# Kernel tuning notes

Measured on AMD Instinct MI355X. Metric: run time of the kernel, lower is better.

## Reference

```python
import jax, jax.numpy as jnp
import numpy as np

B, S, H, E, K, NH = 2, 2048, 1024, 8, 2, 8
HD = H // NH          # head dim = 128
HQ = H // 4           # seasonal encoder width = 256
CAP = int(B * S * 1.5 * K / E)  # expert capacity = 1536


def setup_inputs() -> dict:
    key = jax.random.key(0)
    ks = iter(jax.random.split(key, 32))

    def lin(shape):
        fan_in = shape[0]
        return jax.random.normal(next(ks), shape, jnp.float32) / np.sqrt(fan_in)

    inp = {
        "hidden_states": jax.random.normal(next(ks), (B, S, H), jnp.float32),
        # position embedding table [sequence_length, H]
        "pos_emb": jax.random.normal(next(ks), (S, H), jnp.float32) * 0.02,
        # temporal_encoder: Linear(H+2,H) -> ReLU -> Linear(H,H)
        "We1": lin((H + 2, H)), "be1": jnp.zeros((H,), jnp.float32),
        "We2": lin((H, H)),     "be2": jnp.zeros((H,), jnp.float32),
        # seasonal_encoder: Linear(1,H//4) -> ReLU -> Linear(H//4,H//4)
        "Ws1": lin((1, HQ)),   "bs1": jnp.zeros((HQ,), jnp.float32),
        "Ws2": lin((HQ, HQ)),  "bs2": jnp.zeros((HQ,), jnp.float32),
        # temporal_attention (MultiheadAttention, 8 heads)
        "Wq": lin((H, H)), "bq": jnp.zeros((H,), jnp.float32),
        "Wk": lin((H, H)), "bk": jnp.zeros((H,), jnp.float32),
        "Wv": lin((H, H)), "bv": jnp.zeros((H,), jnp.float32),
        "Wo": lin((H, H)), "bo": jnp.zeros((H,), jnp.float32),
        # temporal_router: Linear(H,H) -> ReLU -> Linear(H,E)
        "Wr1": lin((H, H)), "br1": jnp.zeros((H,), jnp.float32),
        "Wr2": lin((H, E)), "br2": jnp.zeros((E,), jnp.float32),
    }
    return inp


def _forward(hidden_states, pos_emb, We1, be1, We2, be2, Ws1, bs1, Ws2, bs2,
             Wq, bq, Wk, bk, Wv, bv, Wo, bo, Wr1, br1, Wr2, br2):
    b, s, h = hidden_states.shape
    # time features (time_info is None -> defaults)
    t = jnp.arange(s, dtype=jnp.float32)                   # [S]
    season = jnp.sin(t * 2.0 * jnp.pi / 24.0)              # [S]
    time_feat = jnp.broadcast_to(jnp.stack([t, season], -1), (b, s, 2))

    combined = jnp.concatenate([hidden_states, time_feat], axis=-1)  # [B,S,H+2]
    enc = jax.nn.relu(combined @ We1 + be1) @ We2 + be2              # [B,S,H]

    pos = pos_emb[:s]                                                # [S,H]
    seas = jax.nn.relu(season[:, None] @ Ws1 + bs1) @ Ws2 + bs2      # [S,H//4]
    seas_full = jnp.tile(seas, (1, h // seas.shape[-1]))             # [S,H] (expand to H)

    x = enc + pos[None] + seas_full[None]                            # [B,S,H]

    # self-attention (eval mode, no dropout)
    def heads(y):
        return y.reshape(b, s, NH, HD)
    q = heads(x @ Wq + bq)
    k = heads(x @ Wk + bk)
    v = heads(x @ Wv + bv)
    scores = jnp.einsum('bqhd,bkhd->bhqk', q, k) / np.sqrt(HD)
    attn = jax.nn.softmax(scores, axis=-1)
    ctx = jnp.einsum('bhqk,bkhd->bqhd', attn, v).reshape(b, s, h)
    x = ctx @ Wo + bo

    logits = jax.nn.relu(x @ Wr1 + br1) @ Wr2 + br2                  # [B,S,E]
    probs = jax.nn.softmax(logits, axis=-1)

    topv, topi = jax.lax.top_k(probs, K)                             # [B,S,K]
    topv = topv / topv.sum(-1, keepdims=True)

    onehot = jax.nn.one_hot(topi, E, dtype=probs.dtype)              # [B,S,K,E]
    disp0 = onehot.sum(-2)                                           # [B,S,E] (0/1)
    comb0 = (topv[..., None] * onehot).sum(-2)                       # [B,S,E]

    # only capacity slot 0 is ever written (per original code)
    dispatch = jnp.zeros((b, s, E, CAP), probs.dtype).at[..., 0].set(disp0)
    combine = jnp.zeros((b, s, E, CAP), probs.dtype).at[..., 0].set(comb0)

    p_mean = probs.mean(axis=(0, 1))                                 # [E]
    aux_loss = jnp.sum(p_mean * jnp.log(p_mean * E + 1e-9))
    return dispatch, combine, probs, aux_loss


def reference(hidden_states, pos_emb, We1, be1, We2, be2, Ws1, bs1, Ws2, bs2,
              Wq, bq, Wk, bk, Wv, bv, Wo, bo, Wr1, br1, Wr2, br2):
    return _forward(hidden_states, pos_emb, We1, be1, We2, be2, Ws1, bs1, Ws2, bs2,
                    Wq, bq, Wk, bk, Wv, bv, Wo, bo, Wr1, br1, Wr2, br2)
```

## Files before the change

### kernel.cpp

```cpp
#include <hip/hip_runtime.h>
#include <hip/hip_fp16.h>
#include <math.h>

#define N_TOK 4096
#define S_LEN 2048
#define H_DIM 1024
#define E_EXP 8
#define CAPV  1536
#define NHEAD 8
#define HDHD  128

typedef __attribute__((ext_vector_type(8))) _Float16 v8h;
typedef __attribute__((ext_vector_type(4))) float v4f;

__device__ __forceinline__ void splitf16(float v, unsigned short& h, unsigned short& l) {
    __half hh = __float2half(v);
    h = __half_as_ushort(hh);
    l = __half_as_ushort(__float2half(v - __half2float(hh)));
}

__device__ __forceinline__ void gld_lds16(const void* g, void* l) {
    __builtin_amdgcn_global_load_lds(
        (const __attribute__((address_space(1))) unsigned int*)g,
        (__attribute__((address_space(3))) unsigned int*)l,
        16, 0, 0);
}

__global__ void season_k(float* seasons) {
    int s = blockIdx.x * 256 + threadIdx.x;
    if (s < S_LEN) {
        double a = (double)s * 2.0 * M_PI / 24.0;
        seasons[s] = (float)sin(a);
    }
}

__global__ void seas24_k(const float* __restrict__ seasons,
                         const float* __restrict__ Ws1, const float* __restrict__ bs1,
                         const float* __restrict__ Ws2, const float* __restrict__ bs2,
                         float* __restrict__ seas24) {
    __shared__ float hbuf[256];
    int m = blockIdx.x;
    float sv = seasons[m];
    int j = threadIdx.x;
    hbuf[j] = fmaxf(sv * Ws1[j] + bs1[j], 0.f);
    __syncthreads();
    float acc = bs2[j];
    for (int i = 0; i < 256; ++i) acc = fmaf(hbuf[i], Ws2[i * 256 + j], acc);
    seas24[m * 256 + j] = acc;
}

__global__ void wr2t_k(const float* __restrict__ Wr2, float* __restrict__ Wr2T) {
    int i = blockIdx.x * 256 + threadIdx.x;
    int k = i >> 3, e = i & 7;
    Wr2T[e * 1024 + k] = Wr2[i];
}

__global__ void convert_split_k(const float* __restrict__ in,
                                unsigned short* __restrict__ hi,
                                unsigned short* __restrict__ lo, int n4) {
    int i = blockIdx.x * 256 + threadIdx.x;
    if (i >= n4) return;
    float4 v = ((const float4*)in)[i];
    ushort4 h, l;
    splitf16(v.x, h.x, l.x);
    splitf16(v.y, h.y, l.y);
    splitf16(v.z, h.z, l.z);
    splitf16(v.w, h.w, l.w);
    ((ushort4*)hi)[i] = h;
    ((ushort4*)lo)[i] = l;
}

__device__ __forceinline__ void wconv_body(const float* __restrict__ W,
                                           unsigned short* __restrict__ Thi,
                                           unsigned short* __restrict__ Tlo) {
    __shared__ unsigned short Hs[64][65];
    __shared__ unsigned short Ls[64][65];
    int k0 = blockIdx.y * 64, n0 = blockIdx.x * 64;
    int tid = threadIdx.x;
#pragma unroll
    for (int i = 0; i < 4; ++i) {
        int idx = tid + i * 256;
        int kk = idx >> 4, n4 = idx & 15;
        float4 v = *(const float4*)(W + (size_t)(k0 + kk) * 1024 + n0 + n4 * 4);
        unsigned short h, l;
        splitf16(v.x, h, l); Hs[n4 * 4 + 0][kk] = h; Ls[n4 * 4 + 0][kk] = l;
        splitf16(v.y, h, l); Hs[n4 * 4 + 1][kk] = h; Ls[n4 * 4 + 1][kk] = l;
        splitf16(v.z, h, l); Hs[n4 * 4 + 2][kk] = h; Ls[n4 * 4 + 2][kk] = l;
        splitf16(v.w, h, l); Hs[n4 * 4 + 3][kk] = h; Ls[n4 * 4 + 3][kk] = l;
    }
    __syncthreads();
#pragma unroll
    for (int i = 0; i < 4; ++i) {
        int idx = tid + i * 256;
        int n = idx >> 4, k4 = idx & 15;
        ushort4 h = make_ushort4(Hs[n][k4 * 4], Hs[n][k4 * 4 + 1], Hs[n][k4 * 4 + 2], Hs[n][k4 * 4 + 3]);
        ushort4 l = make_ushort4(Ls[n][k4 * 4], Ls[n][k4 * 4 + 1], Ls[n][k4 * 4 + 2], Ls[n][k4 * 4 + 3]);
        *(ushort4*)(Thi + (size_t)(n0 + n) * 1024 + k0 + k4 * 4) = h;
        *(ushort4*)(Tlo + (size_t)(n0 + n) * 1024 + k0 + k4 * 4) = l;
    }
}

__global__ __launch_bounds__(256) void wconv_t_k(const float* __restrict__ W,
                                                 unsigned short* __restrict__ Thi,
                                                 unsigned short* __restrict__ Tlo) {
    wconv_body(W, Thi, Tlo);
}

struct WBatch {
    const float* src[7];
    unsigned short* dh[7];
    unsigned short* dl[7];
};

__global__ __launch_bounds__(256) void wconv_batch_k(WBatch wb) {
    int i = blockIdx.z;
    wconv_body(wb.src[i], wb.dh[i], wb.dl[i]);
}

template <int MODE, int EMITF, int EMITS, int EMITT>
__global__ __launch_bounds__(256, 2) void gemm_split(
    const unsigned short* __restrict__ Ahi, const unsigned short* __restrict__ Alo,
    const unsigned short* __restrict__ WThi, const unsigned short* __restrict__ WTlo,
    const float* __restrict__ bias, float* __restrict__ Cf,
    unsigned short* __restrict__ Chi, unsigned short* __restrict__ Clo,
    const float* __restrict__ rowT, const float* __restrict__ rowS,
    const float* __restrict__ seasons, const float* __restrict__ pos,
    const float* __restrict__ seas24, float escale) {
    __shared__ unsigned short Ash[2][128 * 32];
    __shared__ unsigned short Asl[2][128 * 32];
    __shared__ unsigned short Bsh[2][64 * 32];
    __shared__ unsigned short Bsl[2][64 * 32];
    int tid = threadIdx.x;
    int lane = tid & 63, w = tid >> 6;
    int l15 = lane & 15, l16 = lane >> 4;
    int wm = (w >> 1) * 64, wn = (w & 1) * 32;
    int m0 = blockIdx.y * 128, n0 = blockIdx.x * 64;

    int ac0 = w * 128 + lane;
    int ac1 = ac0 + 64;
    int bc  = w * 64 + lane;
    int ar0 = ac0 >> 2, ar1 = ac1 >> 2, bn = bc >> 2;
    size_t a_src0 = (size_t)(m0 + ar0) * 1024 + (((ac0 & 3) ^ (ar0 & 3)) * 8);
    size_t a_src1 = (size_t)(m0 + ar1) * 1024 + (((ac1 & 3) ^ (ar1 & 3)) * 8);
    size_t b_src  = (size_t)(n0 + bn) * 1024 + (((bc & 3) ^ (bn & 3)) * 8);

    int a_off[4], b_off[2];
#pragma unroll
    for (int mi = 0; mi < 4; ++mi) {
        int row = wm + mi * 16 + l15;
        a_off[mi] = row * 32 + ((l16 ^ (row & 3)) * 8);
    }
#pragma unroll
    for (int ni = 0; ni < 2; ++ni) {
        int n = wn + ni * 16 + l15;
        b_off[ni] = n * 32 + ((l16 ^ (n & 3)) * 8);
    }

    auto STAGE = [&](int buf, int k0) {
        gld_lds16(Ahi + a_src0 + k0, &Ash[buf][ac0 * 8]);
        gld_lds16(Ahi + a_src1 + k0, &Ash[buf][ac1 * 8]);
        gld_lds16(Alo + a_src0 + k0, &Asl[buf][ac0 * 8]);
        gld_lds16(Alo + a_src1 + k0, &Asl[buf][ac1 * 8]);
        gld_lds16(WThi + b_src + k0, &Bsh[buf][bc * 8]);
        gld_lds16(WTlo + b_src + k0, &Bsl[buf][bc * 8]);
    };

    v4f acc[4][2] = {};
    STAGE(0, 0);
    __syncthreads();

    for (int kk = 0; kk < 32; ++kk) {
        int cur = kk & 1;
        if (kk < 31) STAGE(cur ^ 1, (kk + 1) * 32);
        v8h ah[4], al[4], bh[2], bl[2];
#pragma unroll
        for (int mi = 0; mi < 4; ++mi) {
            ah[mi] = *(const v8h*)&Ash[cur][a_off[mi]];
            al[mi] = *(const v8h*)&Asl[cur][a_off[mi]];
        }
#pragma unroll
        for (int ni = 0; ni < 2; ++ni) {
            bh[ni] = *(const v8h*)&Bsh[cur][b_off[ni]];
            bl[ni] = *(const v8h*)&Bsl[cur][b_off[ni]];
        }
#pragma unroll
        for (int mi = 0; mi < 4; ++mi)
#pragma unroll
            for (int ni = 0; ni < 2; ++ni) {
                acc[mi][ni] = __builtin_amdgcn_mfma_f32_16x16x32_f16(ah[mi], bh[ni], acc[mi][ni], 0, 0, 0);
                acc[mi][ni] = __builtin_amdgcn_mfma_f32_16x16x32_f16(al[mi], bh[ni], acc[mi][ni], 0, 0, 0);
                acc[mi][ni] = __builtin_amdgcn_mfma_f32_16x16x32_f16(ah[mi], bl[ni], acc[mi][ni], 0, 0, 0);
            }
        __syncthreads();
    }

    if (EMITT) {
#pragma unroll
        for (int mi = 0; mi < 4; ++mi) {
            int row0 = m0 + wm + mi * 16 + l16 * 4;
            int bb = row0 >> 11, ss = row0 & 2047;
#pragma unroll
            for (int ni = 0; ni < 2; ++ni) {
                int col = n0 + wn + ni * 16 + l15;
                int hh = col >> 7, dd = col & 127;
                size_t base = ((size_t)((bb * 8 + hh) * 128 + dd)) * 2048 + ss;
                ushort4 vh, vl;
                float v0 = acc[mi][ni][0] + bias[col];
                float v1 = acc[mi][ni][1] + bias[col];
                float v2 = acc[mi][ni][2] + bias[col];
                float v3 = acc[mi][ni][3] + bias[col];
                splitf16(v0, vh.x, vl.x);
                splitf16(v1, vh.y, vl.y);
                splitf16(v2, vh.z, vl.z);
                splitf16(v3, vh.w, vl.w);
                *(ushort4*)(Chi + base) = vh;
                *(ushort4*)(Clo + base) = vl;
            }
        }
    } else {
#pragma unroll
        for (int mi = 0; mi < 4; ++mi) {
#pragma unroll
            for (int r = 0; r < 4; ++r) {
                int row = m0 + wm + mi * 16 + l16 * 4 + r;
                int s = row & (S_LEN - 1);
                float tval = 0.f, seval = 0.f;
                if (MODE == 1) { tval = (float)s; seval = seasons[s]; }
#pragma unroll
                for (int ni = 0; ni < 2; ++ni) {
                    int col = n0 + wn + ni * 16 + l15;
                    float v = acc[mi][ni][r] + bias[col];
                    if (MODE == 1) v += tval * rowT[col] + seval * rowS[col];
                    if (MODE == 2) v += pos[(size_t)s * 1024 + col] + seas24[(s % 24) * 256 + (col & 255)];
                    if (MODE == 1 || MODE == 3) v = fmaxf(v, 0.f);
                    size_t o = (size_t)row * 1024 + col;
                    if (EMITF) Cf[o] = v;
                    if (EMITS) {
                        unsigned short hu, lu;
                        splitf16(v * escale, hu, lu);
                        Chi[o] = hu; Clo[o] = lu;
                    }
                }
            }
        }
    }
}

#define ATTN_LDS_BYTES (4 * 2 * 4096 * 2 + 64 * 32 * 4)

__global__ __launch_bounds__(256, 2) void attn_mfma_k(
    const unsigned short* __restrict__ qhi, const unsigned short* __restrict__ qlo,
    const unsigned short* __restrict__ khi, const unsigned short* __restrict__ klo,
    const unsigned short* __restrict__ vthi, const unsigned short* __restrict__ vtlo,
    unsigned short* __restrict__ ctx_hi, unsigned short* __restrict__ ctx_lo) {
    extern __shared__ char smem_raw[];
    unsigned short* Ks_hi = (unsigned short*)smem_raw;
    unsigned short* Ks_lo = Ks_hi + 2 * 4096;
    unsigned short* Vs_hi = Ks_lo + 2 * 4096;
    unsigned short* Vs_lo = Vs_hi + 2 * 4096;
    unsigned int*   Ps    = (unsigned int*)(Vs_lo + 2 * 4096);

    int bh = blockIdx.y;
    int b = bh >> 3, h = bh & 7;
    int q0 = blockIdx.x * 64;
    int tid = threadIdx.x;
    int lane = tid & 63, w = tid >> 6;
    int l15 = lane & 15, l16 = lane >> 4;
    int wm = w * 16;

    v8h qa_h[4], qa_l[4];
    {
        size_t qrow = (size_t)(b * S_LEN + q0 + wm + l15) * H_DIM + h * HDHD;
#pragma unroll
        for (int ks = 0; ks < 4; ++ks) {
            qa_h[ks] = *(const v8h*)(qhi + qrow + ks * 32 + l16 * 8);
            qa_l[ks] = *(const v8h*)(qlo + qrow + ks * 32 + l16 * 8);
        }
    }

    int ktok1 = tid >> 4, kslot1 = tid & 15;
    int ktok2 = ktok1 + 16;
    size_t ksrc1 = (size_t)(b * S_LEN + ktok1) * H_DIM + h * HDHD + ((kslot1 ^ (ktok1 & 7)) * 8);
    size_t ksrc2 = (size_t)(b * S_LEN + ktok2) * H_DIM + h * HDHD + ((kslot1 ^ (ktok2 & 7)) * 8);
    int vd1 = tid >> 2, vslot1 = tid & 3;
    int vd2 = vd1 + 64;
    size_t vsrc1 = (size_t)(bh * HDHD + vd1) * S_LEN + ((vslot1 ^ ((vd1 >> 1) & 3)) * 8);
    size_t vsrc2 = (size_t)(bh * HDHD + vd2) * S_LEN + ((vslot1 ^ ((vd2 >> 1) & 3)) * 8);

    auto STAGE = [&](int buf, int kt) {
        size_t koff = (size_t)kt * H_DIM;
        int o = buf * 4096;
        gld_lds16(khi + ksrc1 + koff, &Ks_hi[o + tid * 8]);
        gld_lds16(khi + ksrc2 + koff, &Ks_hi[o + (tid + 256) * 8]);
        gld_lds16(klo + ksrc1 + koff, &Ks_lo[o + tid * 8]);
        gld_lds16(klo + ksrc2 + koff, &Ks_lo[o + (tid + 256) * 8]);
        gld_lds16(vthi + vsrc1 + kt, &Vs_hi[o + tid * 8]);
        gld_lds16(vthi + vsrc2 + kt, &Vs_hi[o + (tid + 256) * 8]);
        gld_lds16(vtlo + vsrc1 + kt, &Vs_lo[o + tid * 8]);
        gld_lds16(vtlo + vsrc2 + kt, &Vs_lo[o + (tid + 256) * 8]);
    };

    v4f accO[8] = {};
    float mreg[4] = {-1e30f, -1e30f, -1e30f, -1e30f};
    float lreg[4] = {};

    STAGE(0, 0);
    __syncthreads();

    for (int it = 0; it < 64; ++it) {
        int cur = it & 1;
        int co = cur * 4096;
        if (it < 63) STAGE(cur ^ 1, (it + 1) * 32);

        v4f s0 = {}, s1 = {};
#pragma unroll
        for (int ks = 0; ks < 4; ++ks) {
#pragma unroll
            for (int nt = 0; nt < 2; ++nt) {
                int tok = nt * 16 + l15;
                int slot = (ks * 4 + l16) ^ (tok & 7);
                v8h bhf = *(const v8h*)&Ks_hi[co + tok * 128 + slot * 8];
                v8h blf = *(const v8h*)&Ks_lo[co + tok * 128 + slot * 8];
                v4f& ss = nt ? s1 : s0;
                ss = __builtin_amdgcn_mfma_f32_16x16x32_f16(qa_h[ks], bhf, ss, 0, 0, 0);
                ss = __builtin_amdgcn_mfma_f32_16x16x32_f16(qa_l[ks], bhf, ss, 0, 0, 0);
                ss = __builtin_amdgcn_mfma_f32_16x16x32_f16(qa_h[ks], blf, ss, 0, 0, 0);
            }
        }

        float p0[4], p1[4], alpha[4];
#pragma unroll
        for (int r = 0; r < 4; ++r) {
            float tmax = fmaxf(s0[r], s1[r]);
            tmax = fmaxf(tmax, __shfl_xor(tmax, 1));
            tmax = fmaxf(tmax, __shfl_xor(tmax, 2));
            tmax = fmaxf(tmax, __shfl_xor(tmax, 4));
            tmax = fmaxf(tmax, __shfl_xor(tmax, 8));
            float mnew = fmaxf(mreg[r], tmax);
            alpha[r] = __expf(mreg[r] - mnew);
            p0[r] = __expf(s0[r] - mnew);
            p1[r] = __expf(s1[r] - mnew);
            float lt = p0[r] + p1[r];
            lt += __shfl_xor(lt, 1);
            lt += __shfl_xor(lt, 2);
            lt += __shfl_xor(lt, 4);
            lt += __shfl_xor(lt, 8);
            lreg[r] = lreg[r] * alpha[r] + lt;
            mreg[r] = mnew;
        }
#pragma unroll
        for (int nt = 0; nt < 8; ++nt)
#pragma unroll
            for (int r = 0; r < 4; ++r) accO[nt][r] *= alpha[r];

#pragma unroll
        for (int r = 0; r < 4; ++r) {
            int qq = wm + l16 * 4 + r;
            unsigned short ph, pl;
            splitf16(p0[r], ph, pl);
            int k0i = l15;
            Ps[qq * 32 + ((((k0i >> 2) ^ (qq & 7)) << 2) | (k0i & 3))] =
                (unsigned)ph | ((unsigned)pl << 16);
            splitf16(p1[r], ph, pl);
            int k1i = 16 + l15;
            Ps[qq * 32 + ((((k1i >> 2) ^ (qq & 7)) << 2) | (k1i & 3))] =
                (unsigned)ph | ((unsigned)pl << 16);
        }

        int qq = wm + l15;
        int sA = (l16 * 2) ^ (qq & 7);
        int sB = (l16 * 2 + 1) ^ (qq & 7);
        uint4 ua = *(const uint4*)&Ps[qq * 32 + sA * 4];
        uint4 ub = *(const uint4*)&Ps[qq * 32 + sB * 4];
        uint4 ahw, alw;
        ahw.x = (ua.x & 0xffffu) | (ua.y << 16);
        ahw.y = (ua.z & 0xffffu) | (ua.w << 16);
        ahw.z = (ub.x & 0xffffu) | (ub.y << 16);
        ahw.w = (ub.z & 0xffffu) | (ub.w << 16);
        alw.x = (ua.x >> 16) | (ua.y & 0xffff0000u);
        alw.y = (ua.z >> 16) | (ua.w & 0xffff0000u);
        alw.z = (ub.x >> 16) | (ub.y & 0xffff0000u);
        alw.w = (ub.z >> 16) | (ub.w & 0xffff0000u);
        v8h pA_h = __builtin_bit_cast(v8h, ahw);
        v8h pA_l = __builtin_bit_cast(v8h, alw);
#pragma unroll
        for (int nt = 0; nt < 8; ++nt) {
            int d = nt * 16 + l15;
            int slot = l16 ^ ((d >> 1) & 3);
            v8h vhf = *(const v8h*)&Vs_hi[co + d * 32 + slot * 8];
            v8h vlf = *(const v8h*)&Vs_lo[co + d * 32 + slot * 8];
            accO[nt] = __builtin_amdgcn_mfma_f32_16x16x32_f16(pA_h, vhf, accO[nt], 0, 0, 0);
            accO[nt] = __builtin_amdgcn_mfma_f32_16x16x32_f16(pA_l, vhf, accO[nt], 0, 0, 0);
            accO[nt] = __builtin_amdgcn_mfma_f32_16x16x32_f16(pA_h, vlf, accO[nt], 0, 0, 0);
        }
        __syncthreads();
    }

    float linv[4];
#pragma unroll
    for (int r = 0; r < 4; ++r) linv[r] = 1.f / lreg[r];
#pragma unroll
    for (int nt = 0; nt < 8; ++nt) {
#pragma unroll
        for (int r = 0; r < 4; ++r) {
            size_t o = (size_t)(b * S_LEN + q0 + wm + l16 * 4 + r) * H_DIM + h * HDHD + nt * 16 + l15;
            unsigned short hu, lu;
            splitf16(accO[nt][r] * linv[r], hu, lu);
            ctx_hi[o] = hu;
            ctx_lo[o] = lu;
        }
    }
}

__global__ __launch_bounds__(256) void logits_k(const float* __restrict__ h1,
                                                const float* __restrict__ Wr2T,
                                                const float* __restrict__ br2,
                                                float* __restrict__ logits) {
    __shared__ float part[256];
    int tid = threadIdx.x;
    int tok8 = tid >> 5;
    int e = (tid >> 2) & 7;
    int ch = tid & 3;
    int tok = blockIdx.x * 8 + tok8;
    const float4* h4 = (const float4*)(h1 + (size_t)tok * 1024 + ch * 256);
    const float4* w4 = (const float4*)(Wr2T + (size_t)e * 1024 + ch * 256);
    float acc = 0.f;
#pragma unroll
    for (int i = 0; i < 64; ++i) {
        float4 a = h4[i];
        float4 bb = w4[i];
        acc = fmaf(a.x, bb.x, fmaf(a.y, bb.y, fmaf(a.z, bb.z, fmaf(a.w, bb.w, acc))));
    }
    part[tid] = acc;
    __syncthreads();
    if (ch == 0) {
        float s = part[tid] + part[tid + 1] + part[tid + 2] + part[tid + 3] + br2[e];
        logits[(size_t)tok * 8 + e] = s;
    }
}

__global__ __launch_bounds__(256) void topk_fill_k(const float* __restrict__ logits,
                                                   float* __restrict__ out) {
    int tok = blockIdx.x;
    int tid = threadIdx.x;
    float l[8], p[8];
    float mx = -1e30f;
#pragma unroll
    for (int e = 0; e < 8; ++e) { l[e] = logits[(size_t)tok * 8 + e]; mx = fmaxf(mx, l[e]); }
    float sum = 0.f;
#pragma unroll
    for (int e = 0; e < 8; ++e) { p[e] = __expf(l[e] - mx); sum += p[e]; }
    float inv = 1.f / sum;
#pragma unroll
    for (int e = 0; e < 8; ++e) p[e] *= inv;
    int i1 = 0;
#pragma unroll
    for (int e = 1; e < 8; ++e) if (p[e] > p[i1]) i1 = e;
    int i2 = -1;
#pragma unroll
    for (int e = 0; e < 8; ++e) {
        if (e == i1) continue;
        if (i2 < 0 || p[e] > p[i2]) i2 = e;
    }
    float tv = p[i1] + p[i2];
    float w1 = p[i1] / tv, w2 = p[i2] / tv;

    const size_t NEC = (size_t)N_TOK * E_EXP * CAPV;
    v4f* dbase = (v4f*)(out + (size_t)tok * E_EXP * CAPV);
    v4f* cbase = (v4f*)(out + NEC + (size_t)tok * E_EXP * CAPV);
    const int NF4 = E_EXP * CAPV / 4;
#pragma unroll
    for (int it = 0; it < NF4 / 256; ++it) {
        int f = it * 256 + tid;
        int e = f / (CAPV / 4);
        int c4 = f - e * (CAPV / 4);
        v4f dv = {0.f, 0.f, 0.f, 0.f};
        v4f cv = {0.f, 0.f, 0.f, 0.f};
        if (c4 == 0) {
            if (e == i1) { dv[0] = 1.f; cv[0] = w1; }
            else if (e == i2) { dv[0] = 1.f; cv[0] = w2; }
        }
        __builtin_nontemporal_store(dv, dbase + f);
        __builtin_nontemporal_store(cv, cbase + f);
    }
    if (tid < 2) {
        float4 pv = tid == 0 ? make_float4(p[0], p[1], p[2], p[3])
                             : make_float4(p[4], p[5], p[6], p[7]);
        ((float4*)(out + 2 * NEC + (size_t)tok * 8))[tid] = pv;
    }
}

__global__ void aux_k(const float* __restrict__ probs, float* __restrict__ out_aux) {
    __shared__ float part[256];
    int tid = threadIdx.x;
    int e = tid & 7, chunk = tid >> 3;
    float s = 0.f;
    for (int t = chunk * 128; t < (chunk + 1) * 128; ++t)
        s += probs[(size_t)t * 8 + e];
    part[tid] = s;
    __syncthreads();
    if (tid < 8) {
        float tot = 0.f;
        for (int c = 0; c < 32; ++c) tot += part[c * 8 + e];
        part[tid] = tot / (float)N_TOK;
    }
    __syncthreads();
    if (tid == 0) {
        float aux = 0.f;
        for (int e2 = 0; e2 < 8; ++e2) {
            float pm = part[e2];
            aux += pm * logf(pm * 8.f + 1e-9f);
        }
        *out_aux = aux;
    }
}

extern "C" void kernel_launch(void* const* d_in, const int* in_sizes, int n_in,
                              void* d_out, int out_size, void* d_ws, size_t ws_size,
                              hipStream_t stream) {
    const float* hid = (const float*)d_in[0];
    const float* pos = (const float*)d_in[1];
    const float* We1 = (const float*)d_in[2];
    const float* be1 = (const float*)d_in[3];
    const float* We2 = (const float*)d_in[4];
    const float* be2 = (const float*)d_in[5];
    const float* Ws1 = (const float*)d_in[6];
    const float* bs1 = (const float*)d_in[7];
    const float* Ws2 = (const float*)d_in[8];
    const float* bs2 = (const float*)d_in[9];
    const float* Wq  = (const float*)d_in[10]; const float* bq = (const float*)d_in[11];
    const float* Wk  = (const float*)d_in[12]; const float* bk = (const float*)d_in[13];
    const float* Wv  = (const float*)d_in[14]; const float* bv = (const float*)d_in[15];
    const float* Wo  = (const float*)d_in[16]; const float* bo = (const float*)d_in[17];
    const float* Wr1 = (const float*)d_in[18]; const float* br1 = (const float*)d_in[19];
    const float* Wr2 = (const float*)d_in[20]; const float* br2 = (const float*)d_in[21];

    float* out = (float*)d_out;
    char* base = (char*)d_ws;
    const size_t AC  = (size_t)N_TOK * H_DIM;
    const size_t SPC = AC * 2;
    const size_t FB  = AC * 4;
    const size_t WSZ = (size_t)1024 * 1024 * 4;

    unsigned short* B1hi = (unsigned short*)(base);
    unsigned short* B1lo = (unsigned short*)(base + SPC);
    unsigned short* B2hi = (unsigned short*)(base + FB);
    unsigned short* B2lo = (unsigned short*)(base + FB + SPC);
    unsigned short* Qhi  = (unsigned short*)(base + 2 * FB);
    unsigned short* Qlo  = (unsigned short*)(base + 2 * FB + SPC);
    unsigned short* Khi  = (unsigned short*)(base + 3 * FB);
    unsigned short* Klo  = (unsigned short*)(base + 3 * FB + SPC);
    unsigned short* VThi = (unsigned short*)(base + 4 * FB);
    unsigned short* VTlo = (unsigned short*)(base + 4 * FB + SPC);
    float* h1f = (float*)(base + 3 * FB);

    char* wbase = base + 5 * FB;
    bool batched = ws_size >= 5 * FB + 7 * WSZ + (1u << 20);
    unsigned short* Whi[7];
    unsigned short* Wlo[7];
    for (int i = 0; i < 7; ++i) {
        size_t off = batched ? (size_t)i * WSZ : 0;
        Whi[i] = (unsigned short*)(wbase + off);
        Wlo[i] = (unsigned short*)(wbase + off + WSZ / 2);
    }
    char* smalls = wbase + (batched ? 7 * WSZ : WSZ);
    float* wr2t    = (float*)smalls;
    float* seas24  = wr2t + 8192;
    float* seasons = seas24 + 6144;
    float* logits  = seasons + 2048;

    const size_t NEC = (size_t)N_TOK * E_EXP * CAPV;
    const float QSCALE = 0.08838834764831845f;

    static bool attr_set = false;
    if (!attr_set) {
        hipFuncSetAttribute((const void*)attn_mfma_k,
                            hipFuncAttributeMaxDynamicSharedMemorySize,
                            ATTN_LDS_BYTES);
        attr_set = true;
    }

    dim3 gg(16, 32), blk(256);
    dim3 wg(16, 16);

    season_k<<<8, 256, 0, stream>>>(seasons);
    seas24_k<<<24, 256, 0, stream>>>(seasons, Ws1, bs1, Ws2, bs2, seas24);
    wr2t_k<<<32, 256, 0, stream>>>(Wr2, wr2t);
    convert_split_k<<<4096, 256, 0, stream>>>(hid, B1hi, B1lo, (int)(AC / 4));

    const float* wsrc[7] = {We1, We2, Wq, Wk, Wv, Wo, Wr1};
    if (batched) {
        WBatch wb;
        for (int i = 0; i < 7; ++i) { wb.src[i] = wsrc[i]; wb.dh[i] = Whi[i]; wb.dl[i] = Wlo[i]; }
        wconv_batch_k<<<dim3(16, 16, 7), blk, 0, stream>>>(wb);
    }

    auto conv = [&](int i) {
        if (!batched) wconv_t_k<<<wg, blk, 0, stream>>>(wsrc[i], Whi[i], Wlo[i]);
    };

    conv(0);
    gemm_split<1, 0, 1, 0><<<gg, blk, 0, stream>>>(B1hi, B1lo, Whi[0], Wlo[0], be1,
        nullptr, B2hi, B2lo,
        We1 + (size_t)1024 * 1024, We1 + (size_t)1025 * 1024, seasons, nullptr, nullptr, 1.f);
    conv(1);
    gemm_split<2, 0, 1, 0><<<gg, blk, 0, stream>>>(B2hi, B2lo, Whi[1], Wlo[1], be2,
        nullptr, B1hi, B1lo, nullptr, nullptr, nullptr, pos, seas24, 1.f);
    conv(2);
    gemm_split<0, 0, 1, 0><<<gg, blk, 0, stream>>>(B1hi, B1lo, Whi[2], Wlo[2], bq,
        nullptr, Qhi, Qlo, nullptr, nullptr, nullptr, nullptr, nullptr, QSCALE);
    conv(3);
    gemm_split<0, 0, 1, 0><<<gg, blk, 0, stream>>>(B1hi, B1lo, Whi[3], Wlo[3], bk,
        nullptr, Khi, Klo, nullptr, nullptr, nullptr, nullptr, nullptr, 1.f);
    conv(4);
    gemm_split<0, 0, 0, 1><<<gg, blk, 0, stream>>>(B1hi, B1lo, Whi[4], Wlo[4], bv,
        nullptr, VThi, VTlo, nullptr, nullptr, nullptr, nullptr, nullptr, 1.f);

    attn_mfma_k<<<dim3(32, 16), 256, ATTN_LDS_BYTES, stream>>>(Qhi, Qlo, Khi, Klo,
                                                               VThi, VTlo, B2hi, B2lo);

    conv(5);
    gemm_split<0, 0, 1, 0><<<gg, blk, 0, stream>>>(B2hi, B2lo, Whi[5], Wlo[5], bo,
        nullptr, B1hi, B1lo, nullptr, nullptr, nullptr, nullptr, nullptr, 1.f);
    conv(6);
    gemm_split<3, 1, 0, 0><<<gg, blk, 0, stream>>>(B1hi, B1lo, Whi[6], Wlo[6], br1,
        h1f, nullptr, nullptr, nullptr, nullptr, nullptr, nullptr, nullptr, 1.f);

    logits_k<<<512, 256, 0, stream>>>(h1f, wr2t, br2, logits);
    topk_fill_k<<<4096, 256, 0, stream>>>(logits, out);
    aux_k<<<1, 256, 0, stream>>>(out + 2 * NEC, out + 2 * NEC + (size_t)N_TOK * E_EXP);
}
```

Baseline: 626.8 us.

## Rewrite flash attention with 32x32 MFMA tiles and larger query/key blocks

Rebuilds the attention kernel around 32x32x16 MFMA instructions. Each block now covers 128 queries, with 32 per wave, and each iteration processes 64 keys. The V hi/lo halves are interleaved into a single swizzled LDS buffer and the P@V step is done in two phases. The aim is more reuse of each staged K/V tile and fewer loop iterations and barriers. In exchange the grid shrinks to 256 blocks at one block per CU with much more LDS and register pressure, which may leave CUs idle or underoccupied.

```diff
diff --git a/kernel.cpp b/kernel.cpp
--- a/kernel.cpp
+++ b/kernel.cpp
@@ -12,6 +12,7 @@
 
 typedef __attribute__((ext_vector_type(8))) _Float16 v8h;
 typedef __attribute__((ext_vector_type(4))) float v4f;
+typedef __attribute__((ext_vector_type(16))) float v16f;
 
 __device__ __forceinline__ void splitf16(float v, unsigned short& h, unsigned short& l) {
     __half hh = __float2half(v);
@@ -246,166 +247,186 @@
     }
 }
 
-#define ATTN_LDS_BYTES (4 * 2 * 4096 * 2 + 64 * 32 * 4)
-
-__global__ __launch_bounds__(256, 2) void attn_mfma_k(
+#define ATTN_LDS_BYTES (2 * (16384 + 16384 + 32768) + 16384)
+
+__global__ __launch_bounds__(256, 1) void attn_mfma_k(
     const unsigned short* __restrict__ qhi, const unsigned short* __restrict__ qlo,
     const unsigned short* __restrict__ khi, const unsigned short* __restrict__ klo,
     const unsigned short* __restrict__ vthi, const unsigned short* __restrict__ vtlo,
     unsigned short* __restrict__ ctx_hi, unsigned short* __restrict__ ctx_lo) {
     extern __shared__ char smem_raw[];
     unsigned short* Ks_hi = (unsigned short*)smem_raw;
-    unsigned short* Ks_lo = Ks_hi + 2 * 4096;
-    unsigned short* Vs_hi = Ks_lo + 2 * 4096;
-    unsigned short* Vs_lo = Vs_hi + 2 * 4096;
-    unsigned int*   Ps    = (unsigned int*)(Vs_lo + 2 * 4096);
+    unsigned short* Ks_lo = Ks_hi + 2 * 8192;
+    unsigned short* Vs    = Ks_lo + 2 * 8192;
+    unsigned int*   Ps    = (unsigned int*)(Vs + 2 * 16384);
 
     int bh = blockIdx.y;
     int b = bh >> 3, h = bh & 7;
-    int q0 = blockIdx.x * 64;
+    int q0 = blockIdx.x * 128;
     int tid = threadIdx.x;
     int lane = tid & 63, w = tid >> 6;
-    int l15 = lane & 15, l16 = lane >> 4;
-    int wm = w * 16;
-
-    v8h qa_h[4], qa_l[4];
+    int l31 = lane & 31, g = lane >> 5;
+
+    v8h qa_h[8], qa_l[8];
     {
-        size_t qrow = (size_t)(b * S_LEN + q0 + wm + l15) * H_DIM + h * HDHD;
-#pragma unroll
-        for (int ks = 0; ks < 4; ++ks) {
-            qa_h[ks] = *(const v8h*)(qhi + qrow + ks * 32 + l16 * 8);
-            qa_l[ks] = *(const v8h*)(qlo + qrow + ks * 32 + l16 * 8);
-        }
-    }
-
-    int ktok1 = tid >> 4, kslot1 = tid & 15;
-    int ktok2 = ktok1 + 16;
-    size_t ksrc1 = (size_t)(b * S_LEN + ktok1) * H_DIM + h * HDHD + ((kslot1 ^ (ktok1 & 7)) * 8);
-    size_t ksrc2 = (size_t)(b * S_LEN + ktok2) * H_DIM + h * HDHD + ((kslot1 ^ (ktok2 & 7)) * 8);
-    int vd1 = tid >> 2, vslot1 = tid & 3;
-    int vd2 = vd1 + 64;
-    size_t vsrc1 = (size_t)(bh * HDHD + vd1) * S_LEN + ((vslot1 ^ ((vd1 >> 1) & 3)) * 8);
-    size_t vsrc2 = (size_t)(bh * HDHD + vd2) * S_LEN + ((vslot1 ^ ((vd2 >> 1) & 3)) * 8);
+        size_t qrow = (size_t)(b * S_LEN + q0 + w * 32 + l31) * H_DIM + h * HDHD + g * 8;
+#pragma unroll
+        for (int ks = 0; ks < 8; ++ks) {
+            qa_h[ks] = *(const v8h*)(qhi + qrow + ks * 16);
+            qa_l[ks] = *(const v8h*)(qlo + qrow + ks * 16);
+        }
+    }
+
+    size_t kbase[4]; int kdst[4];
+#pragma unroll
+    for (int r = 0; r < 4; ++r) {
+        int c = tid + r * 256;
+        int tok = c >> 4, slot = c & 15;
+        kbase[r] = (size_t)(b * S_LEN + tok) * H_DIM + h * HDHD + ((slot ^ (tok & 15)) * 8);
+        kdst[r] = c * 8;
+    }
+    const unsigned short* vsrc[8]; int vdst[8];
+#pragma unroll
+    for (int r = 0; r < 8; ++r) {
+        int c = tid + r * 256;
+        int d = c >> 4, slot = c & 15;
+        int logical = slot ^ (d & 15);
+        int p = logical >> 3, tokc = logical & 7;
+        vsrc[r] = (p ? vtlo : vthi) + (size_t)(bh * HDHD + d) * S_LEN + tokc * 8;
+        vdst[r] = c * 8;
+    }
 
     auto STAGE = [&](int buf, int kt) {
+        int ko = buf * 8192, vo = buf * 16384;
         size_t koff = (size_t)kt * H_DIM;
-        int o = buf * 4096;
-        gld_lds16(khi + ksrc1 + koff, &Ks_hi[o + tid * 8]);
-        gld_lds16(khi + ksrc2 + koff, &Ks_hi[o + (tid + 256) * 8]);
-        gld_lds16(klo + ksrc1 + koff, &Ks_lo[o + tid * 8]);
-        gld_lds16(klo + ksrc2 + koff, &Ks_lo[o + (tid + 256) * 8]);
-        gld_lds16(vthi + vsrc1 + kt, &Vs_hi[o + tid * 8]);
-        gld_lds16(vthi + vsrc2 + kt, &Vs_hi[o + (tid + 256) * 8]);
-        gld_lds16(vtlo + vsrc1 + kt, &Vs_lo[o + tid * 8]);
-        gld_lds16(vtlo + vsrc2 + kt, &Vs_lo[o + (tid + 256) * 8]);
+#pragma unroll
+        for (int r = 0; r < 4; ++r) {
+            gld_lds16(khi + kbase[r] + koff, &Ks_hi[ko + kdst[r]]);
+            gld_lds16(klo + kbase[r] + koff, &Ks_lo[ko + kdst[r]]);
+        }
+#pragma unroll
+        for (int r = 0; r < 8; ++r)
+            gld_lds16(vsrc[r] + kt, &Vs[vo + vdst[r]]);
     };
 
-    v4f accO[8] = {};
-    float mreg[4] = {-1e30f, -1e30f, -1e30f, -1e30f};
-    float lreg[4] = {};
+    v16f O[4] = {};
+    float mreg[16], lreg[16];
+#pragma unroll
+    for (int i = 0; i < 16; ++i) { mreg[i] = -1e30f; lreg[i] = 0.f; }
 
     STAGE(0, 0);
     __syncthreads();
 
-    for (int it = 0; it < 64; ++it) {
+    for (int it = 0; it < 32; ++it) {
         int cur = it & 1;
-        int co = cur * 4096;
-        if (it < 63) STAGE(cur ^ 1, (it + 1) * 32);
-
-        v4f s0 = {}, s1 = {};
-#pragma unroll
-        for (int ks = 0; ks < 4; ++ks) {
-#pragma unroll
-            for (int nt = 0; nt < 2; ++nt) {
-                int tok = nt * 16 + l15;
-                int slot = (ks * 4 + l16) ^ (tok & 7);
-                v8h bhf = *(const v8h*)&Ks_hi[co + tok * 128 + slot * 8];
-                v8h blf = *(const v8h*)&Ks_lo[co + tok * 128 + slot * 8];
-                v4f& ss = nt ? s1 : s0;
-                ss = __builtin_amdgcn_mfma_f32_16x16x32_f16(qa_h[ks], bhf, ss, 0, 0, 0);
-                ss = __builtin_amdgcn_mfma_f32_16x16x32_f16(qa_l[ks], bhf, ss, 0, 0, 0);
-                ss = __builtin_amdgcn_mfma_f32_16x16x32_f16(qa_h[ks], blf, ss, 0, 0, 0);
+        if (it < 31) STAGE(cur ^ 1, (it + 1) * 64);
+        int ko = cur * 8192, vo = cur * 16384;
+
+        v16f s0 = {}, s1 = {};
+#pragma unroll
+        for (int ks = 0; ks < 8; ++ks) {
+            int slot = ks * 2 + g;
+#pragma unroll
+            for (int j = 0; j < 2; ++j) {
+                int tok = j * 32 + l31;
+                int a = ko + tok * 128 + ((slot ^ (tok & 15)) * 8);
+                v8h kh = *(const v8h*)&Ks_hi[a];
+                v8h kl = *(const v8h*)&Ks_lo[a];
+                if (j == 0) {
+                    s0 = __builtin_amdgcn_mfma_f32_32x32x16_f16(qa_h[ks], kh, s0, 0, 0, 0);
+                    s0 = __builtin_amdgcn_mfma_f32_32x32x16_f16(qa_l[ks], kh, s0, 0, 0, 0);
+                    s0 = __builtin_amdgcn_mfma_f32_32x32x16_f16(qa_h[ks], kl, s0, 0, 0, 0);
+                } else {
+                    s1 = __builtin_amdgcn_mfma_f32_32x32x16_f16(qa_h[ks], kh, s1, 0, 0, 0);
+                    s1 = __builtin_amdgcn_mfma_f32_32x32x16_f16(qa_l[ks], kh, s1, 0, 0, 0);
+                    s1 = __builtin_amdgcn_mfma_f32_32x32x16_f16(qa_h[ks], kl, s1, 0, 0, 0);
+                }
             }
         }
 
-        float p0[4], p1[4], alpha[4];
-#pragma unroll
-        for (int r = 0; r < 4; ++r) {
-            float tmax = fmaxf(s0[r], s1[r]);
-            tmax = fmaxf(tmax, __shfl_xor(tmax, 1));
-            tmax = fmaxf(tmax, __shfl_xor(tmax, 2));
-            tmax = fmaxf(tmax, __shfl_xor(tmax, 4));
-            tmax = fmaxf(tmax, __shfl_xor(tmax, 8));
-            float mnew = fmaxf(mreg[r], tmax);
-            alpha[r] = __expf(mreg[r] - mnew);
-            p0[r] = __expf(s0[r] - mnew);
-            p1[r] = __expf(s1[r] - mnew);
-            float lt = p0[r] + p1[r];
+        float p0a[16], p1a[16], alpha[16];
+#pragma unroll
+        for (int i = 0; i < 16; ++i) {
+            float rm = fmaxf(s0[i], s1[i]);
+            rm = fmaxf(rm, __shfl_xor(rm, 1));
+            rm = fmaxf(rm, __shfl_xor(rm, 2));
+            rm = fmaxf(rm, __shfl_xor(rm, 4));
+            rm = fmaxf(rm, __shfl_xor(rm, 8));
+            rm = fmaxf(rm, __shfl_xor(rm, 16));
+            float mnew = fmaxf(mreg[i], rm);
+            alpha[i] = __expf(mreg[i] - mnew);
+            p0a[i] = __expf(s0[i] - mnew);
+            p1a[i] = __expf(s1[i] - mnew);
+            float lt = p0a[i] + p1a[i];
             lt += __shfl_xor(lt, 1);
             lt += __shfl_xor(lt, 2);
             lt += __shfl_xor(lt, 4);
             lt += __shfl_xor(lt, 8);
-            lreg[r] = lreg[r] * alpha[r] + lt;
-            mreg[r] = mnew;
-        }
-#pragma unroll
-        for (int nt = 0; nt < 8; ++nt)
-#pragma unroll
-            for (int r = 0; r < 4; ++r) accO[nt][r] *= alpha[r];
-
-#pragma unroll
-        for (int r = 0; r < 4; ++r) {
-            int qq = wm + l16 * 4 + r;
-            unsigned short ph, pl;
-            splitf16(p0[r], ph, pl);
-            int k0i = l15;
-            Ps[qq * 32 + ((((k0i >> 2) ^ (qq & 7)) << 2) | (k0i & 3))] =
-                (unsigned)ph | ((unsigned)pl << 16);
-            splitf16(p1[r], ph, pl);
-            int k1i = 16 + l15;
-            Ps[qq * 32 + ((((k1i >> 2) ^ (qq & 7)) << 2) | (k1i & 3))] =
-                (unsigned)ph | ((unsigned)pl << 16);
-        }
-
-        int qq = wm + l15;
-        int sA = (l16 * 2) ^ (qq & 7);
-        int sB = (l16 * 2 + 1) ^ (qq & 7);
-        uint4 ua = *(const uint4*)&Ps[qq * 32 + sA * 4];
-        uint4 ub = *(const uint4*)&Ps[qq * 32 + sB * 4];
-        uint4 ahw, alw;
-        ahw.x = (ua.x & 0xffffu) | (ua.y << 16);
-        ahw.y = (ua.z & 0xffffu) | (ua.w << 16);
-        ahw.z = (ub.x & 0xffffu) | (ub.y << 16);
-        ahw.w = (ub.z & 0xffffu) | (ub.w << 16);
-        alw.x = (ua.x >> 16) | (ua.y & 0xffff0000u);
-        alw.y = (ua.z >> 16) | (ua.w & 0xffff0000u);
-        alw.z = (ub.x >> 16) | (ub.y & 0xffff0000u);
-        alw.w = (ub.z >> 16) | (ub.w & 0xffff0000u);
-        v8h pA_h = __builtin_bit_cast(v8h, ahw);
-        v8h pA_l = __builtin_bit_cast(v8h, alw);
-#pragma unroll
-        for (int nt = 0; nt < 8; ++nt) {
-            int d = nt * 16 + l15;
-            int slot = l16 ^ ((d >> 1) & 3);
-            v8h vhf = *(const v8h*)&Vs_hi[co + d * 32 + slot * 8];
-            v8h vlf = *(const v8h*)&Vs_lo[co + d * 32 + slot * 8];
-            accO[nt] = __builtin_amdgcn_mfma_f32_16x16x32_f16(pA_h, vhf, accO[nt], 0, 0, 0);
-            accO[nt] = __builtin_amdgcn_mfma_f32_16x16x32_f16(pA_l, vhf, accO[nt], 0, 0, 0);
-            accO[nt] = __builtin_amdgcn_mfma_f32_16x16x32_f16(pA_h, vlf, accO[nt], 0, 0, 0);
+            lt += __shfl_xor(lt, 16);
+            lreg[i] = lreg[i] * alpha[i] + lt;
+            mreg[i] = mnew;
+        }
+#pragma unroll
+        for (int t = 0; t < 4; ++t)
+#pragma unroll
+            for (int i = 0; i < 16; ++i) O[t][i] *= alpha[i];
+
+#pragma unroll
+        for (int ph = 0; ph < 2; ++ph) {
+#pragma unroll
+            for (int i = 0; i < 16; ++i) {
+                int R = w * 32 + (i & 3) + 8 * (i >> 2) + 4 * g;
+                unsigned short phh, pll;
+                splitf16(ph == 0 ? p0a[i] : p1a[i], phh, pll);
+                int t32 = l31;
+                Ps[R * 32 + ((((t32 >> 2) ^ (R & 7)) << 2) | (t32 & 3))] =
+                    (unsigned)phh | ((unsigned)pll << 16);
+            }
+            int R = w * 32 + l31;
+#pragma unroll
+            for (int ks2 = 0; ks2 < 2; ++ks2) {
+                int s0i = ks2 * 4 + g * 2;
+                uint4 ua = *(const uint4*)&Ps[R * 32 + ((s0i ^ (R & 7)) * 4)];
+                uint4 ub = *(const uint4*)&Ps[R * 32 + (((s0i + 1) ^ (R & 7)) * 4)];
+                uint4 ahw, alw;
+                ahw.x = (ua.x & 0xffffu) | (ua.y << 16);
+                ahw.y = (ua.z & 0xffffu) | (ua.w << 16);
+                ahw.z = (ub.x & 0xffffu) | (ub.y << 16);
+                ahw.w = (ub.z & 0xffffu) | (ub.w << 16);
+                alw.x = (ua.x >> 16) | (ua.y & 0xffff0000u);
+                alw.y = (ua.z >> 16) | (ua.w & 0xffff0000u);
+                alw.z = (ub.x >> 16) | (ub.y & 0xffff0000u);
+                alw.w = (ub.z >> 16) | (ub.w & 0xffff0000u);
+                v8h pA_h = __builtin_bit_cast(v8h, ahw);
+                v8h pA_l = __builtin_bit_cast(v8h, alw);
+                int gks = ph * 2 + ks2;
+#pragma unroll
+                for (int t = 0; t < 4; ++t) {
+                    int d = t * 32 + l31;
+                    int sh = gks * 2 + g;
+                    int sl = 8 + gks * 2 + g;
+                    v8h vh = *(const v8h*)&Vs[vo + d * 128 + ((sh ^ (d & 15)) * 8)];
+                    v8h vl = *(const v8h*)&Vs[vo + d * 128 + ((sl ^ (d & 15)) * 8)];
+                    O[t] = __builtin_amdgcn_mfma_f32_32x32x16_f16(pA_h, vh, O[t], 0, 0, 0);
+                    O[t] = __builtin_amdgcn_mfma_f32_32x32x16_f16(pA_l, vh, O[t], 0, 0, 0);
+                    O[t] = __builtin_amdgcn_mfma_f32_32x32x16_f16(pA_h, vl, O[t], 0, 0, 0);
+                }
+            }
         }
         __syncthreads();
     }
 
-    float linv[4];
-#pragma unroll
-    for (int r = 0; r < 4; ++r) linv[r] = 1.f / lreg[r];
-#pragma unroll
-    for (int nt = 0; nt < 8; ++nt) {
-#pragma unroll
-        for (int r = 0; r < 4; ++r) {
-            size_t o = (size_t)(b * S_LEN + q0 + wm + l16 * 4 + r) * H_DIM + h * HDHD + nt * 16 + l15;
+    float linv[16];
+#pragma unroll
+    for (int i = 0; i < 16; ++i) linv[i] = 1.f / lreg[i];
+#pragma unroll
+    for (int t = 0; t < 4; ++t) {
+#pragma unroll
+        for (int i = 0; i < 16; ++i) {
+            int q = q0 + w * 32 + (i & 3) + 8 * (i >> 2) + 4 * g;
+            size_t o = (size_t)(b * S_LEN + q) * H_DIM + h * HDHD + t * 32 + l31;
             unsigned short hu, lu;
-            splitf16(accO[nt][r] * linv[r], hu, lu);
+            splitf16(O[t][i] * linv[i], hu, lu);
             ctx_hi[o] = hu;
             ctx_lo[o] = lu;
         }
@@ -616,7 +637,7 @@
     gemm_split<0, 0, 0, 1><<<gg, blk, 0, stream>>>(B1hi, B1lo, Whi[4], Wlo[4], bv,
         nullptr, VThi, VTlo, nullptr, nullptr, nullptr, nullptr, nullptr, 1.f);
 
-    attn_mfma_k<<<dim3(32, 16), 256, ATTN_LDS_BYTES, stream>>>(Qhi, Qlo, Khi, Klo,
+    attn_mfma_k<<<dim3(16, 16), 256, ATTN_LDS_BYTES, stream>>>(Qhi, Qlo, Khi, Klo,
                                                                VThi, VTlo, B2hi, B2lo);
 
     conv(5);
```

New measurement: 680.0 us. 1.08x slower.

## Split attention over key halves with a combine kernel, and fuse prep kernels

Applied to the files above, without the earlier changes.

Attention is now split along the key dimension into two halves (flash-decoding style). Each half writes unnormalized partial outputs plus its running max and sum into scratch space in the output buffer, and a new combine kernel merges the halves and emits the hi/lo fp16 context. The attention kernel now single-buffers its LDS tiles with static shared memory and targets 4 blocks per CU, trading the copy/compute overlap for more occupancy and twice as many blocks. The four small preprocessing kernels are also merged into a single launch, removing launch overhead.

```diff
diff --git a/kernel.cpp b/kernel.cpp
--- a/kernel.cpp
+++ b/kernel.cpp
@@ -26,48 +26,47 @@
         16, 0, 0);
 }
 
-__global__ void season_k(float* seasons) {
-    int s = blockIdx.x * 256 + threadIdx.x;
-    if (s < S_LEN) {
-        double a = (double)s * 2.0 * M_PI / 24.0;
-        seasons[s] = (float)sin(a);
-    }
-}
-
-__global__ void seas24_k(const float* __restrict__ seasons,
-                         const float* __restrict__ Ws1, const float* __restrict__ bs1,
-                         const float* __restrict__ Ws2, const float* __restrict__ bs2,
-                         float* __restrict__ seas24) {
+__global__ __launch_bounds__(256) void prep_k(
+    const float* __restrict__ hid, unsigned short* __restrict__ hi,
+    unsigned short* __restrict__ lo,
+    const float* __restrict__ Ws1, const float* __restrict__ bs1,
+    const float* __restrict__ Ws2, const float* __restrict__ bs2,
+    float* __restrict__ seasons, float* __restrict__ seas24,
+    const float* __restrict__ Wr2, float* __restrict__ wr2t) {
     __shared__ float hbuf[256];
-    int m = blockIdx.x;
-    float sv = seasons[m];
-    int j = threadIdx.x;
-    hbuf[j] = fmaxf(sv * Ws1[j] + bs1[j], 0.f);
-    __syncthreads();
-    float acc = bs2[j];
-    for (int i = 0; i < 256; ++i) acc = fmaf(hbuf[i], Ws2[i * 256 + j], acc);
-    seas24[m * 256 + j] = acc;
-}
-
-__global__ void wr2t_k(const float* __restrict__ Wr2, float* __restrict__ Wr2T) {
-    int i = blockIdx.x * 256 + threadIdx.x;
-    int k = i >> 3, e = i & 7;
-    Wr2T[e * 1024 + k] = Wr2[i];
-}
-
-__global__ void convert_split_k(const float* __restrict__ in,
-                                unsigned short* __restrict__ hi,
-                                unsigned short* __restrict__ lo, int n4) {
-    int i = blockIdx.x * 256 + threadIdx.x;
-    if (i >= n4) return;
-    float4 v = ((const float4*)in)[i];
-    ushort4 h, l;
-    splitf16(v.x, h.x, l.x);
-    splitf16(v.y, h.y, l.y);
-    splitf16(v.z, h.z, l.z);
-    splitf16(v.w, h.w, l.w);
-    ((ushort4*)hi)[i] = h;
-    ((ushort4*)lo)[i] = l;
+    int blk = blockIdx.x;
+    int tid = threadIdx.x;
+    if (blk < 4096) {
+        int i = blk * 256 + tid;
+        float4 v = ((const float4*)hid)[i];
+        ushort4 h, l;
+        splitf16(v.x, h.x, l.x);
+        splitf16(v.y, h.y, l.y);
+        splitf16(v.z, h.z, l.z);
+        splitf16(v.w, h.w, l.w);
+        ((ushort4*)hi)[i] = h;
+        ((ushort4*)lo)[i] = l;
+    } else if (blk < 4104) {
+        int s = (blk - 4096) * 256 + tid;
+        if (s < S_LEN) {
+            double a = (double)s * 2.0 * M_PI / 24.0;
+            seasons[s] = (float)sin(a);
+        }
+    } else if (blk < 4128) {
+        int m = blk - 4104;
+        double a = (double)m * 2.0 * M_PI / 24.0;
+        float sv = (float)sin(a);
+        int j = tid;
+        hbuf[j] = fmaxf(sv * Ws1[j] + bs1[j], 0.f);
+        __syncthreads();
+        float acc = bs2[j];
+        for (int i = 0; i < 256; ++i) acc = fmaf(hbuf[i], Ws2[i * 256 + j], acc);
+        seas24[m * 256 + j] = acc;
+    } else {
+        int i = (blk - 4128) * 256 + tid;
+        int k = i >> 3, e = i & 7;
+        wr2t[e * 1024 + k] = Wr2[i];
+    }
 }
 
 __device__ __forceinline__ void wconv_body(const float* __restrict__ W,
@@ -246,23 +245,21 @@
     }
 }
 
-#define ATTN_LDS_BYTES (4 * 2 * 4096 * 2 + 64 * 32 * 4)
-
-__global__ __launch_bounds__(256, 2) void attn_mfma_k(
+__global__ __launch_bounds__(256, 4) void attn_mfma_k(
     const unsigned short* __restrict__ qhi, const unsigned short* __restrict__ qlo,
     const unsigned short* __restrict__ khi, const unsigned short* __restrict__ klo,
     const unsigned short* __restrict__ vthi, const unsigned short* __restrict__ vtlo,
-    unsigned short* __restrict__ ctx_hi, unsigned short* __restrict__ ctx_lo) {
-    extern __shared__ char smem_raw[];
-    unsigned short* Ks_hi = (unsigned short*)smem_raw;
-    unsigned short* Ks_lo = Ks_hi + 2 * 4096;
-    unsigned short* Vs_hi = Ks_lo + 2 * 4096;
-    unsigned short* Vs_lo = Vs_hi + 2 * 4096;
-    unsigned int*   Ps    = (unsigned int*)(Vs_lo + 2 * 4096);
+    float* __restrict__ OP, float* __restrict__ ML) {
+    __shared__ unsigned short Ks_hi[32 * 128];
+    __shared__ unsigned short Ks_lo[32 * 128];
+    __shared__ unsigned short Vs_hi[128 * 32];
+    __shared__ unsigned short Vs_lo[128 * 32];
+    __shared__ unsigned int   Ps[64 * 32];
 
     int bh = blockIdx.y;
     int b = bh >> 3, h = bh & 7;
     int q0 = blockIdx.x * 64;
+    int z = blockIdx.z;
     int tid = threadIdx.x;
     int lane = tid & 63, w = tid >> 6;
     int l15 = lane & 15, l16 = lane >> 4;
@@ -287,30 +284,24 @@
     size_t vsrc1 = (size_t)(bh * HDHD + vd1) * S_LEN + ((vslot1 ^ ((vd1 >> 1) & 3)) * 8);
     size_t vsrc2 = (size_t)(bh * HDHD + vd2) * S_LEN + ((vslot1 ^ ((vd2 >> 1) & 3)) * 8);
 
-    auto STAGE = [&](int buf, int kt) {
-        size_t koff = (size_t)kt * H_DIM;
-        int o = buf * 4096;
-        gld_lds16(khi + ksrc1 + koff, &Ks_hi[o + tid * 8]);
-        gld_lds16(khi + ksrc2 + koff, &Ks_hi[o + (tid + 256) * 8]);
-        gld_lds16(klo + ksrc1 + koff, &Ks_lo[o + tid * 8]);
-        gld_lds16(klo + ksrc2 + koff, &Ks_lo[o + (tid + 256) * 8]);
-        gld_lds16(vthi + vsrc1 + kt, &Vs_hi[o + tid * 8]);
-        gld_lds16(vthi + vsrc2 + kt, &Vs_hi[o + (tid + 256) * 8]);
-        gld_lds16(vtlo + vsrc1 + kt, &Vs_lo[o + tid * 8]);
-        gld_lds16(vtlo + vsrc2 + kt, &Vs_lo[o + (tid + 256) * 8]);
-    };
-
     v4f accO[8] = {};
     float mreg[4] = {-1e30f, -1e30f, -1e30f, -1e30f};
     float lreg[4] = {};
 
-    STAGE(0, 0);
-    __syncthreads();
-
-    for (int it = 0; it < 64; ++it) {
-        int cur = it & 1;
-        int co = cur * 4096;
-        if (it < 63) STAGE(cur ^ 1, (it + 1) * 32);
+    int kt0 = z * 1024;
+    for (int it = 0; it < 32; ++it) {
+        int kt = kt0 + it * 32;
+        __syncthreads();
+        size_t koff = (size_t)kt * H_DIM;
+        gld_lds16(khi + ksrc1 + koff, &Ks_hi[tid * 8]);
+        gld_lds16(khi + ksrc2 + koff, &Ks_hi[(tid + 256) * 8]);
+        gld_lds16(klo + ksrc1 + koff, &Ks_lo[tid * 8]);
+        gld_lds16(klo + ksrc2 + koff, &Ks_lo[(tid + 256) * 8]);
+        gld_lds16(vthi + vsrc1 + kt, &Vs_hi[tid * 8]);
+        gld_lds16(vthi + vsrc2 + kt, &Vs_hi[(tid + 256) * 8]);
+        gld_lds16(vtlo + vsrc1 + kt, &Vs_lo[tid * 8]);
+        gld_lds16(vtlo + vsrc2 + kt, &Vs_lo[(tid + 256) * 8]);
+        __syncthreads();
 
         v4f s0 = {}, s1 = {};
 #pragma unroll
@@ -319,8 +310,8 @@
             for (int nt = 0; nt < 2; ++nt) {
                 int tok = nt * 16 + l15;
                 int slot = (ks * 4 + l16) ^ (tok & 7);
-                v8h bhf = *(const v8h*)&Ks_hi[co + tok * 128 + slot * 8];
-                v8h blf = *(const v8h*)&Ks_lo[co + tok * 128 + slot * 8];
+                v8h bhf = *(const v8h*)&Ks_hi[tok * 128 + slot * 8];
+                v8h blf = *(const v8h*)&Ks_lo[tok * 128 + slot * 8];
                 v4f& ss = nt ? s1 : s0;
                 ss = __builtin_amdgcn_mfma_f32_16x16x32_f16(qa_h[ks], bhf, ss, 0, 0, 0);
                 ss = __builtin_amdgcn_mfma_f32_16x16x32_f16(qa_l[ks], bhf, ss, 0, 0, 0);
@@ -387,29 +378,69 @@
         for (int nt = 0; nt < 8; ++nt) {
             int d = nt * 16 + l15;
             int slot = l16 ^ ((d >> 1) & 3);
-            v8h vhf = *(const v8h*)&Vs_hi[co + d * 32 + slot * 8];
-            v8h vlf = *(const v8h*)&Vs_lo[co + d * 32 + slot * 8];
+            v8h vhf = *(const v8h*)&Vs_hi[d * 32 + slot * 8];
+            v8h vlf = *(const v8h*)&Vs_lo[d * 32 + slot * 8];
             accO[nt] = __builtin_amdgcn_mfma_f32_16x16x32_f16(pA_h, vhf, accO[nt], 0, 0, 0);
             accO[nt] = __builtin_amdgcn_mfma_f32_16x16x32_f16(pA_l, vhf, accO[nt], 0, 0, 0);
             accO[nt] = __builtin_amdgcn_mfma_f32_16x16x32_f16(pA_h, vlf, accO[nt], 0, 0, 0);
         }
-        __syncthreads();
-    }
-
-    float linv[4];
-#pragma unroll
-    for (int r = 0; r < 4; ++r) linv[r] = 1.f / lreg[r];
+    }
+
+#pragma unroll
+    for (int r = 0; r < 4; ++r) {
+        if (l15 == 0) {
+            int q = q0 + wm + l16 * 4 + r;
+            size_t mlo = ((size_t)(z * 16 + bh) * 2048 + q) * 2;
+            ML[mlo] = mreg[r];
+            ML[mlo + 1] = lreg[r];
+        }
+    }
 #pragma unroll
     for (int nt = 0; nt < 8; ++nt) {
 #pragma unroll
         for (int r = 0; r < 4; ++r) {
-            size_t o = (size_t)(b * S_LEN + q0 + wm + l16 * 4 + r) * H_DIM + h * HDHD + nt * 16 + l15;
-            unsigned short hu, lu;
-            splitf16(accO[nt][r] * linv[r], hu, lu);
-            ctx_hi[o] = hu;
-            ctx_lo[o] = lu;
-        }
-    }
+            int q = q0 + wm + l16 * 4 + r;
+            size_t o = ((size_t)(z * 16 + bh) * 2048 + q) * 128 + nt * 16 + l15;
+            OP[o] = accO[nt][r];
+        }
+    }
+}
+
+__global__ __launch_bounds__(256) void attn_combine_k(
+    const float* __restrict__ OP, const float* __restrict__ ML,
+    unsigned short* __restrict__ ctx_hi, unsigned short* __restrict__ ctx_lo) {
+    int tid = threadIdx.x;
+    int R = blockIdx.x * 16 + (tid >> 4);
+    int bh = R >> 11, q = R & 2047;
+    int b = bh >> 3, h = bh & 7;
+    int d0 = (tid & 15) * 8;
+    size_t ml0 = ((size_t)bh * 2048 + q) * 2;
+    size_t ml1 = ((size_t)(16 + bh) * 2048 + q) * 2;
+    float m0 = ML[ml0], l0 = ML[ml0 + 1];
+    float m1 = ML[ml1], l1 = ML[ml1 + 1];
+    float m = fmaxf(m0, m1);
+    float w0 = __expf(m0 - m), w1 = __expf(m1 - m);
+    float inv = 1.f / (w0 * l0 + w1 * l1);
+    const float* O0 = OP + ((size_t)bh * 2048 + q) * 128 + d0;
+    const float* O1 = OP + ((size_t)(16 + bh) * 2048 + q) * 128 + d0;
+    size_t dst = ((size_t)(b * 2048 + q)) * 1024 + h * 128 + d0;
+    float4 a0 = *(const float4*)O0;
+    float4 a1 = *(const float4*)(O0 + 4);
+    float4 c0 = *(const float4*)O1;
+    float4 c1 = *(const float4*)(O1 + 4);
+    ushort4 h0, h1, lo0, lo1;
+    splitf16((w0 * a0.x + w1 * c0.x) * inv, h0.x, lo0.x);
+    splitf16((w0 * a0.y + w1 * c0.y) * inv, h0.y, lo0.y);
+    splitf16((w0 * a0.z + w1 * c0.z) * inv, h0.z, lo0.z);
+    splitf16((w0 * a0.w + w1 * c0.w) * inv, h0.w, lo0.w);
+    splitf16((w0 * a1.x + w1 * c1.x) * inv, h1.x, lo1.x);
+    splitf16((w0 * a1.y + w1 * c1.y) * inv, h1.y, lo1.y);
+    splitf16((w0 * a1.z + w1 * c1.z) * inv, h1.z, lo1.z);
+    splitf16((w0 * a1.w + w1 * c1.w) * inv, h1.w, lo1.w);
+    *(ushort4*)(ctx_hi + dst) = h0;
+    *(ushort4*)(ctx_hi + dst + 4) = h1;
+    *(ushort4*)(ctx_lo + dst) = lo0;
+    *(ushort4*)(ctx_lo + dst + 4) = lo1;
 }
 
 __global__ __launch_bounds__(256) void logits_k(const float* __restrict__ h1,
@@ -572,21 +603,14 @@
     const size_t NEC = (size_t)N_TOK * E_EXP * CAPV;
     const float QSCALE = 0.08838834764831845f;
 
-    static bool attr_set = false;
-    if (!attr_set) {
-        hipFuncSetAttribute((const void*)attn_mfma_k,
-                            hipFuncAttributeMaxDynamicSharedMemorySize,
-                            ATTN_LDS_BYTES);
-        attr_set = true;
-    }
+    float* OP = out;
+    float* ML = out + (size_t)2 * 16 * 2048 * 128;
 
     dim3 gg(16, 32), blk(256);
     dim3 wg(16, 16);
 
-    season_k<<<8, 256, 0, stream>>>(seasons);
-    seas24_k<<<24, 256, 0, stream>>>(seasons, Ws1, bs1, Ws2, bs2, seas24);
-    wr2t_k<<<32, 256, 0, stream>>>(Wr2, wr2t);
-    convert_split_k<<<4096, 256, 0, stream>>>(hid, B1hi, B1lo, (int)(AC / 4));
+    prep_k<<<4160, 256, 0, stream>>>(hid, B1hi, B1lo, Ws1, bs1, Ws2, bs2,
+                                     seasons, seas24, Wr2, wr2t);
 
     const float* wsrc[7] = {We1, We2, Wq, Wk, Wv, Wo, Wr1};
     if (batched) {
@@ -616,8 +640,9 @@
     gemm_split<0, 0, 0, 1><<<gg, blk, 0, stream>>>(B1hi, B1lo, Whi[4], Wlo[4], bv,
         nullptr, VThi, VTlo, nullptr, nullptr, nullptr, nullptr, nullptr, 1.f);
 
-    attn_mfma_k<<<dim3(32, 16), 256, ATTN_LDS_BYTES, stream>>>(Qhi, Qlo, Khi, Klo,
-                                                               VThi, VTlo, B2hi, B2lo);
+    attn_mfma_k<<<dim3(32, 16, 2), 256, 0, stream>>>(Qhi, Qlo, Khi, Klo,
+                                                     VThi, VTlo, OP, ML);
+    attn_combine_k<<<2048, 256, 0, stream>>>(OP, ML, B2hi, B2lo);
 
     conv(5);
     gemm_split<0, 0, 1, 0><<<gg, blk, 0, stream>>>(B2hi, B2lo, Whi[5], Wlo[5], bo,
```

New measurement: 616.4 us. No clear change (-1.7%).
